# Kernel tuning notes

Measured on AMD Instinct MI355X. Metric: run time of the kernel, lower is better.

## Reference

```python
import jax, jax.numpy as jnp
import numpy as np

D_MODEL = 2048
NUM_HEADS = 16
D_K = D_MODEL // NUM_HEADS


def setup_inputs() -> dict:
    key = jax.random.key(0)
    ks = jax.random.split(key, 9)
    s = 1.0 / np.sqrt(D_MODEL)
    return {
        "x": jax.random.normal(ks[0], (2, 2048, D_MODEL), dtype=jnp.float32),
        "Wq": jax.random.normal(ks[1], (D_MODEL, D_MODEL), dtype=jnp.float32) * s,
        "bq": jax.random.normal(ks[2], (D_MODEL,), dtype=jnp.float32) * 0.01,
        "Wk": jax.random.normal(ks[3], (D_MODEL, D_MODEL), dtype=jnp.float32) * s,
        "bk": jax.random.normal(ks[4], (D_MODEL,), dtype=jnp.float32) * 0.01,
        "Wv": jax.random.normal(ks[5], (D_MODEL, D_MODEL), dtype=jnp.float32) * s,
        "bv": jax.random.normal(ks[6], (D_MODEL,), dtype=jnp.float32) * 0.01,
        "Wo": jax.random.normal(ks[7], (D_MODEL, D_MODEL), dtype=jnp.float32) * s,
        "bo": jax.random.normal(ks[8], (D_MODEL,), dtype=jnp.float32) * 0.01,
    }


def reference(x, Wq, bq, Wk, bk, Wv, bv, Wo, bo):
    B, T, C = x.shape
    H, Dk = NUM_HEADS, D_K
    # projections (torch Linear: y = x @ W^T + b; here weights stored as [in,out])
    q = (x @ Wq + bq).reshape(B, T, H, Dk).transpose(0, 2, 1, 3)  # [B,H,T,Dk]
    k = (x @ Wk + bk).reshape(B, T, H, Dk).transpose(0, 2, 1, 3)
    v = (x @ Wv + bv).reshape(B, T, H, Dk).transpose(0, 2, 1, 3)
    score = jnp.einsum("bhqd,bhkd->bhqk", q, k) / jnp.sqrt(jnp.float32(Dk))
    attn = jax.nn.softmax(score, axis=-1)
    out = jnp.einsum("bhqk,bhkd->bhqd", attn, v)  # [B,H,T,Dk]
    out = out.transpose(0, 2, 1, 3).reshape(B, T, C)
    return out @ Wo + bo
```

## Files before the change

### kernel.cpp

```cpp
#include <hip/hip_runtime.h>
#include <cstdint>

typedef _Float16 f16;
typedef __attribute__((ext_vector_type(4))) _Float16 f16x4;
typedef __attribute__((ext_vector_type(8))) _Float16 f16x8;
typedef __attribute__((ext_vector_type(4))) float f32x4;

#define DM   2048
#define TSEQ 2048
#define NB   2
#define NH   16
#define DKH  128
#define LOG2E 1.44269504088896f

__device__ __forceinline__ void gload_lds16(const void* g, void* l) {
  __builtin_amdgcn_global_load_lds((const __attribute__((address_space(1))) void*)g,
                                   (__attribute__((address_space(3))) void*)l, 16, 0, 0);
}

__global__ __launch_bounds__(256) void cvt_kernel(const float* __restrict__ src,
                                                  f16* __restrict__ dst, int n8) {
  int i = blockIdx.x * 256 + threadIdx.x;
  if (i >= n8) return;
  const float4* s = (const float4*)src + 2 * (size_t)i;
  float4 a = s[0], b = s[1];
  f16x8 o;
  o[0]=(f16)a.x; o[1]=(f16)a.y; o[2]=(f16)a.z; o[3]=(f16)a.w;
  o[4]=(f16)b.x; o[5]=(f16)b.y; o[6]=(f16)b.z; o[7]=(f16)b.w;
  ((f16x8*)dst)[i] = o;
}

__global__ __launch_bounds__(256) void wt_kernel(const float* __restrict__ W0, const float* __restrict__ W1,
                                                 const float* __restrict__ W2, const float* __restrict__ W3,
                                                 f16* __restrict__ Dqkv, f16* __restrict__ Dout) {
  __shared__ f16 S[64 * 80];
  int z = blockIdx.z;
  const float* W = (z == 0) ? W0 : (z == 1) ? W1 : (z == 2) ? W2 : W3;
  f16* D = (z < 3) ? (Dqkv + (size_t)z * DM * DM) : Dout;
  int n0 = blockIdx.x * 64, k0 = blockIdx.y * 64;
  int tid = threadIdx.x;
#pragma unroll
  for (int i = 0; i < 4; i++) {
    int flat = i * 256 + tid;
    int r = flat >> 4, c4 = flat & 15;
    float4 v = *(const float4*)(W + (size_t)(k0 + r) * DM + n0 + c4 * 4);
    S[(c4 * 4 + 0) * 80 + r] = (f16)v.x;
    S[(c4 * 4 + 1) * 80 + r] = (f16)v.y;
    S[(c4 * 4 + 2) * 80 + r] = (f16)v.z;
    S[(c4 * 4 + 3) * 80 + r] = (f16)v.w;
  }
  __syncthreads();
#pragma unroll
  for (int i = 0; i < 2; i++) {
    int flat = i * 256 + tid;
    int nl = flat >> 3, kc = flat & 7;
    f16x8 v = *(const f16x8*)&S[nl * 80 + kc * 8];
    *(f16x8*)(D + (size_t)(n0 + nl) * DM + k0 + kc * 8) = v;
  }
}

template <int MODE>
__global__ __launch_bounds__(256) void gemm_kernel(const f16* __restrict__ A, const f16* __restrict__ Bt,
                                                   const float* __restrict__ b0, const float* __restrict__ b1,
                                                   const float* __restrict__ b2,
                                                   f16* __restrict__ Oh, float* __restrict__ Of) {
  __shared__ f16 As[128 * 32];
  __shared__ f16 Bs[128 * 32];
  const int K = DM;
  int tid = threadIdx.x, l = tid & 63, w = tid >> 6;
  int wm = w >> 1, wn = w & 1;
  int m0 = blockIdx.y * 128, n0 = blockIdx.x * 128;
  f32x4 acc[4][4] = {};

  for (int kt = 0; kt < K / 32; ++kt) {
    __syncthreads();
#pragma unroll
    for (int i = 0; i < 2; i++) {
      int flat = (w * 2 + i) * 64 + l;
      int row = flat >> 2, c = flat & 3;
      int csw = c ^ (row & 3);
      gload_lds16(A  + (size_t)(m0 + row) * K + kt * 32 + csw * 8, &As[(w * 2 + i) * 512]);
      gload_lds16(Bt + (size_t)(n0 + row) * K + kt * 32 + csw * 8, &Bs[(w * 2 + i) * 512]);
    }
    __syncthreads();
    f16x8 af[4], bfr[4];
#pragma unroll
    for (int mi = 0; mi < 4; mi++) {
      int row = wm * 64 + mi * 16 + (l & 15);
      int c = (l >> 4) ^ (row & 3);
      af[mi] = *(const f16x8*)&As[row * 32 + c * 8];
    }
#pragma unroll
    for (int ni = 0; ni < 4; ni++) {
      int row = wn * 64 + ni * 16 + (l & 15);
      int c = (l >> 4) ^ (row & 3);
      bfr[ni] = *(const f16x8*)&Bs[row * 32 + c * 8];
    }
#pragma unroll
    for (int mi = 0; mi < 4; mi++)
#pragma unroll
      for (int ni = 0; ni < 4; ni++)
        acc[mi][ni] = __builtin_amdgcn_mfma_f32_16x16x32_f16(af[mi], bfr[ni], acc[mi][ni], 0, 0, 0);
  }

#pragma unroll
  for (int mi = 0; mi < 4; mi++) {
    int gm = m0 + wm * 64 + mi * 16 + ((l >> 4) << 2);
#pragma unroll
    for (int ni = 0; ni < 4; ni++) {
      int gn = n0 + wn * 64 + ni * 16 + (l & 15);
      if (MODE == 0) {
        int proj = gn >> 11, nn = gn & 2047;
        const float* bp = (proj == 0) ? b0 : (proj == 1) ? b1 : b2;
        float bias = bp[nn];
        int h = nn >> 7, d = nn & 127;
        int b = gm >> 11;
        int t0 = gm & 2047;
        if (proj < 2) {
#pragma unroll
          for (int r = 0; r < 4; r++) {
            Oh[(size_t)proj * ((size_t)NB * NH * TSEQ * DKH) +
               (((size_t)(b * NH + h) * TSEQ + t0 + r) * DKH) + d] = (f16)(acc[mi][ni][r] + bias);
          }
        } else {
          f16x4 pk;
#pragma unroll
          for (int r = 0; r < 4; r++) pk[r] = (f16)(acc[mi][ni][r] + bias);
          *(f16x4*)(Oh + 2ull * ((size_t)NB * NH * TSEQ * DKH) +
                    ((size_t)(b * NH + h) * DKH + d) * TSEQ + t0) = pk;
        }
      } else {
        float bias = b0[gn];
#pragma unroll
        for (int r = 0; r < 4; r++)
          Of[(size_t)(gm + r) * DM + gn] = acc[mi][ni][r] + bias;
      }
    }
  }
}

__global__ __launch_bounds__(256, 2) void attn_kernel(const f16* __restrict__ Qb, const f16* __restrict__ Kb,
                                                      const f16* __restrict__ Vtb, f16* __restrict__ AO) {
  __shared__ f16 Ks[64 * 128];
  __shared__ f16 Vt[128 * 64];
  __shared__ f16 Ps[4][32 * 72];
  int tid = threadIdx.x, l = tid & 63, w = tid >> 6;
  int lo = l & 15, hi = l >> 4;
  int lin = blockIdx.x;
  int xcd = lin & 7, slot = lin >> 3;
  int bh = xcd * 4 + (slot & 3), qt = slot >> 2;
  const float CSC = 0.12753257f;
  const float THR = 62.0f;
  const f16* Qg = Qb + (size_t)bh * TSEQ * DKH;
  const f16* Kg = Kb + (size_t)bh * TSEQ * DKH;
  const f16* Vg = Vtb + (size_t)bh * DKH * TSEQ;

  f16x8 aq[2][4];
#pragma unroll
  for (int hf = 0; hf < 2; hf++) {
    int qrow = qt * 128 + w * 32 + hf * 16 + lo;
#pragma unroll
    for (int c = 0; c < 4; c++)
      aq[hf][c] = *(const f16x8*)(Qg + (size_t)qrow * DKH + c * 32 + (hi << 3));
  }

  f32x4 o[2][8] = {};
  float mrow[2] = {-INFINITY, -INFINITY};
  float lrow[2] = {0.f, 0.f};

  for (int ktile = 0; ktile < TSEQ / 64; ++ktile) {
    __syncthreads();
#pragma unroll
    for (int i = 0; i < 4; i++) {
      int chunk = (w * 4 + i) * 64 + l;
      int rowk = chunk >> 4, c = chunk & 15;
      int csw = c ^ (rowk & 15);
      gload_lds16(Kg + (size_t)(ktile * 64 + rowk) * DKH + csw * 8, &Ks[(w * 4 + i) * 512]);
    }
#pragma unroll
    for (int i = 0; i < 4; i++) {
      int chunk = (w * 4 + i) * 64 + l;
      int d = chunk >> 3, c = chunk & 7;
      int csw = c ^ (d & 7);
      gload_lds16(Vg + (size_t)d * TSEQ + ktile * 64 + csw * 8, &Vt[(w * 4 + i) * 512]);
    }
    __syncthreads();

    f32x4 s[2][4] = {};
    __builtin_amdgcn_s_setprio(1);
#pragma unroll
    for (int ks = 0; ks < 4; ++ks) {
      int ktl = ks * 16 + lo;
#pragma unroll
      for (int c = 0; c < 4; c++) {
        int cc = (c * 4 + hi) ^ lo;
        f16x8 bk = *(const f16x8*)&Ks[ktl * 128 + cc * 8];
        s[0][ks] = __builtin_amdgcn_mfma_f32_16x16x32_f16(bk, aq[0][c], s[0][ks], 0, 0, 0);
        s[1][ks] = __builtin_amdgcn_mfma_f32_16x16x32_f16(bk, aq[1][c], s[1][ks], 0, 0, 0);
      }
    }
    __builtin_amdgcn_s_setprio(0);

#pragma unroll
    for (int hf = 0; hf < 2; hf++) {
      float mk[4];
#pragma unroll
      for (int ks = 0; ks < 4; ks++)
        mk[ks] = fmaxf(fmaxf(s[hf][ks][0], s[hf][ks][1]), fmaxf(s[hf][ks][2], s[hf][ks][3]));
      float mt = fmaxf(fmaxf(mk[0], mk[1]), fmaxf(mk[2], mk[3]));
      mt = fmaxf(mt, __shfl_xor(mt, 16));
      mt = fmaxf(mt, __shfl_xor(mt, 32));

      if (__any(mt > mrow[hf] + THR)) {
        float mn = fmaxf(mrow[hf], mt);
        float al = exp2f((mrow[hf] - mn) * CSC);
        mrow[hf] = mn;
        lrow[hf] *= al;
        float alr[4];
#pragma unroll
        for (int r = 0; r < 4; r++) alr[r] = __shfl(al, (hi << 2) + r);
#pragma unroll
        for (int dsub = 0; dsub < 8; dsub++)
#pragma unroll
          for (int r = 0; r < 4; r++) o[hf][dsub][r] *= alr[r];
      }

      float mCn = -mrow[hf] * CSC;
      float sum = 0.f;
#pragma unroll
      for (int ks = 0; ks < 4; ks++) {
        f16x4 pk;
        float part = 0.f;
#pragma unroll
        for (int r = 0; r < 4; r++) {
          float p = exp2f(__builtin_fmaf(s[hf][ks][r], CSC, mCn));
          pk[r] = (f16)p;
          part += p;
        }
        sum += part;
        *(f16x4*)&Ps[w][(hf * 16 + lo) * 72 + ks * 16 + (hi << 2)] = pk;
      }
      sum += __shfl_xor(sum, 16);
      sum += __shfl_xor(sum, 32);
      lrow[hf] += sum;
    }

    f16x8 pa[2][2];
#pragma unroll
    for (int hf = 0; hf < 2; hf++)
#pragma unroll
      for (int kk = 0; kk < 2; kk++)
        pa[hf][kk] = *(const f16x8*)&Ps[w][(hf * 16 + lo) * 72 + kk * 32 + (hi << 3)];
    __builtin_amdgcn_s_setprio(1);
#pragma unroll
    for (int kk = 0; kk < 2; kk++) {
#pragma unroll
      for (int dsub = 0; dsub < 8; dsub++) {
        int d = dsub * 16 + lo;
        f16x8 vf = *(const f16x8*)&Vt[d * 64 + (((kk * 4 + hi) ^ (d & 7)) << 3)];
        o[0][dsub] = __builtin_amdgcn_mfma_f32_16x16x32_f16(pa[0][kk], vf, o[0][dsub], 0, 0, 0);
        o[1][dsub] = __builtin_amdgcn_mfma_f32_16x16x32_f16(pa[1][kk], vf, o[1][dsub], 0, 0, 0);
      }
    }
    __builtin_amdgcn_s_setprio(0);
  }

  int b = bh >> 4, h = bh & 15;
#pragma unroll
  for (int hf = 0; hf < 2; hf++) {
    float inv = 1.0f / lrow[hf];
    float invr[4];
#pragma unroll
    for (int r = 0; r < 4; r++) invr[r] = __shfl(inv, (hi << 2) + r);
#pragma unroll
    for (int r = 0; r < 4; r++) {
      int t = qt * 128 + w * 32 + hf * 16 + (hi << 2) + r;
      f16* dst = AO + ((size_t)b * TSEQ + t) * DM + h * DKH;
#pragma unroll
      for (int dsub = 0; dsub < 8; dsub++)
        dst[dsub * 16 + lo] = (f16)(o[hf][dsub][r] * invr[r]);
    }
  }
}

extern "C" void kernel_launch(void* const* d_in, const int* in_sizes, int n_in,
                              void* d_out, int out_size, void* d_ws, size_t ws_size,
                              hipStream_t stream) {
  const float* x  = (const float*)d_in[0];
  const float* Wq = (const float*)d_in[1];
  const float* bq = (const float*)d_in[2];
  const float* Wk = (const float*)d_in[3];
  const float* bk = (const float*)d_in[4];
  const float* Wv = (const float*)d_in[5];
  const float* bv = (const float*)d_in[6];
  const float* Wo = (const float*)d_in[7];
  const float* bo = (const float*)d_in[8];

  f16* ws    = (f16*)d_ws;
  f16* xb    = ws;
  f16* WtQKV = ws + 8388608ull;
  f16* WtO   = ws + 20971520ull;
  f16* Q     = ws + 25165824ull;
  f16* Kp    = ws + 33554432ull;
  f16* Vp    = ws + 41943040ull;
  f16* AO    = xb;

  cvt_kernel<<<4096, 256, 0, stream>>>(x, xb, (NB * TSEQ * DM) / 8);
  wt_kernel<<<dim3(32, 32, 4), 256, 0, stream>>>(Wq, Wk, Wv, Wo, WtQKV, WtO);
  gemm_kernel<0><<<dim3(48, 32), 256, 0, stream>>>(xb, WtQKV, bq, bk, bv, Q, nullptr);
  attn_kernel<<<512, 256, 0, stream>>>(Q, Kp, Vp, AO);
  gemm_kernel<1><<<dim3(16, 32), 256, 0, stream>>>(AO, WtO, bo, nullptr, nullptr, nullptr, (float*)d_out);
}
```

Before: 285.8 us.

## Rewrite GEMM as 256x128 double-buffered pipelined kernel with XCD-aware tile swizzle

Replaces the simple single-buffered 128x128, K=32 GEMM with a 512-thread, 256x128 tile, K=64 kernel. It double-buffers LDS and interleaves global-to-LDS staging with per-quarter MFMA phases, using manual s_barrier, waitcnt and setprio. The block index is remapped so neighbouring tiles land on the same XCD for L2 reuse. This targets the load/compute serialization and barrier stalls of the old loop, at the cost of more LDS per block (96KB), fragile hand-placed wait counts, and redundant tail loads.

```diff
diff --git a/kernel.cpp b/kernel.cpp
--- a/kernel.cpp
+++ b/kernel.cpp
@@ -17,6 +17,9 @@
   __builtin_amdgcn_global_load_lds((const __attribute__((address_space(1))) void*)g,
                                    (__attribute__((address_space(3))) void*)l, 16, 0, 0);
 }
+
+#define SBAR()  asm volatile("s_barrier" ::: "memory")
+#define LGKM0() { asm volatile("s_waitcnt lgkmcnt(0)" ::: "memory"); __builtin_amdgcn_sched_barrier(0); }
 
 __global__ __launch_bounds__(256) void cvt_kernel(const float* __restrict__ src,
                                                   f16* __restrict__ dst, int n8) {
@@ -60,47 +63,138 @@
 }
 
 template <int MODE>
-__global__ __launch_bounds__(256) void gemm_kernel(const f16* __restrict__ A, const f16* __restrict__ Bt,
-                                                   const float* __restrict__ b0, const float* __restrict__ b1,
-                                                   const float* __restrict__ b2,
-                                                   f16* __restrict__ Oh, float* __restrict__ Of) {
-  __shared__ f16 As[128 * 32];
-  __shared__ f16 Bs[128 * 32];
+__global__ __launch_bounds__(512, 2) void gemm_kernel(const f16* __restrict__ A, const f16* __restrict__ Bt,
+                                                      const float* __restrict__ b0, const float* __restrict__ b1,
+                                                      const float* __restrict__ b2,
+                                                      f16* __restrict__ Oh, float* __restrict__ Of) {
+  __shared__ __align__(16) f16 As[2][256 * 64];
+  __shared__ __align__(16) f16 Bs[2][128 * 64];
   const int K = DM;
+  const int NT = K / 64;
+  const int NITER = NT / 2;
+  const int NXB = (MODE == 0) ? 48 : 16;
+  const int CPX = (MODE == 0) ? 96 : 32;
   int tid = threadIdx.x, l = tid & 63, w = tid >> 6;
+  int lo = l & 15, hi = l >> 4;
   int wm = w >> 1, wn = w & 1;
-  int m0 = blockIdx.y * 128, n0 = blockIdx.x * 128;
+  int lin = blockIdx.x;
+  int swz = (lin & 7) * CPX + (lin >> 3);
+  int bx = swz % NXB, by = swz / NXB;
+  int m0 = by * 256, n0 = bx * 128;
+
+  const f16* Ag = A + (size_t)m0 * K;
+  const f16* Bg = Bt + (size_t)n0 * K;
+
+  auto stageA = [&](int b, int h, int t) {
+#pragma unroll
+    for (int i = 0; i < 2; i++) {
+      int flat = i * 512 + tid;
+      int row = flat >> 3, c = flat & 7;
+      int csw = c ^ (row & 7);
+      gload_lds16(Ag + (size_t)(h * 128 + row) * K + t * 64 + csw * 8,
+                  &As[b][h * 8192 + i * 4096 + w * 512]);
+    }
+  };
+  auto stageB = [&](int b, int t) {
+#pragma unroll
+    for (int i = 0; i < 2; i++) {
+      int flat = i * 512 + tid;
+      int row = flat >> 3, c = flat & 7;
+      int csw = c ^ (row & 7);
+      gload_lds16(Bg + (size_t)row * K + t * 64 + csw * 8,
+                  &Bs[b][i * 4096 + w * 512]);
+    }
+  };
+
   f32x4 acc[4][4] = {};
-
-  for (int kt = 0; kt < K / 32; ++kt) {
-    __syncthreads();
-#pragma unroll
-    for (int i = 0; i < 2; i++) {
-      int flat = (w * 2 + i) * 64 + l;
-      int row = flat >> 2, c = flat & 3;
-      int csw = c ^ (row & 3);
-      gload_lds16(A  + (size_t)(m0 + row) * K + kt * 32 + csw * 8, &As[(w * 2 + i) * 512]);
-      gload_lds16(Bt + (size_t)(n0 + row) * K + kt * 32 + csw * 8, &Bs[(w * 2 + i) * 512]);
-    }
-    __syncthreads();
-    f16x8 af[4], bfr[4];
-#pragma unroll
-    for (int mi = 0; mi < 4; mi++) {
-      int row = wm * 64 + mi * 16 + (l & 15);
-      int c = (l >> 4) ^ (row & 3);
-      af[mi] = *(const f16x8*)&As[row * 32 + c * 8];
-    }
-#pragma unroll
-    for (int ni = 0; ni < 4; ni++) {
-      int row = wn * 64 + ni * 16 + (l & 15);
-      int c = (l >> 4) ^ (row & 3);
-      bfr[ni] = *(const f16x8*)&Bs[row * 32 + c * 8];
-    }
-#pragma unroll
-    for (int mi = 0; mi < 4; mi++)
-#pragma unroll
-      for (int ni = 0; ni < 4; ni++)
-        acc[mi][ni] = __builtin_amdgcn_mfma_f32_16x16x32_f16(af[mi], bfr[ni], acc[mi][ni], 0, 0, 0);
+  f16x8 bfr[4][2];
+
+#define READ_BFRAGS(b)                                                          \
+  {                                                                             \
+    _Pragma("unroll")                                                           \
+    for (int ni = 0; ni < 4; ni++) {                                            \
+      int row = wn * 64 + ni * 16 + lo;                                         \
+      bfr[ni][0] = *(const f16x8*)&Bs[b][row * 64 + (((0 + hi) ^ (row & 7)) << 3)]; \
+      bfr[ni][1] = *(const f16x8*)&Bs[b][row * 64 + (((4 + hi) ^ (row & 7)) << 3)]; \
+    }                                                                           \
+  }
+
+#define PHASE_HEAD(bq, q)                                                       \
+    f16x8 af0, af1;                                                             \
+    {                                                                           \
+      int row = wm * 64 + (q) * 16 + lo;                                        \
+      af0 = *(const f16x8*)&As[bq][row * 64 + (((0 + hi) ^ (row & 7)) << 3)];   \
+      af1 = *(const f16x8*)&As[bq][row * 64 + (((4 + hi) ^ (row & 7)) << 3)];   \
+    }
+
+#define PHASE_MFMA(q)                                                           \
+    __builtin_amdgcn_s_setprio(1);                                              \
+    _Pragma("unroll")                                                           \
+    for (int ni = 0; ni < 4; ni++) {                                            \
+      acc[q][ni] = __builtin_amdgcn_mfma_f32_16x16x32_f16(af0, bfr[ni][0], acc[q][ni], 0, 0, 0); \
+      acc[q][ni] = __builtin_amdgcn_mfma_f32_16x16x32_f16(af1, bfr[ni][1], acc[q][ni], 0, 0, 0); \
+    }                                                                           \
+    __builtin_amdgcn_s_setprio(0);
+
+  stageB(0, 0);
+  stageA(0, 0, 0);
+  stageA(0, 1, 0);
+  stageB(1, 1);
+  asm volatile("s_waitcnt vmcnt(2)" ::: "memory");
+  SBAR();
+
+#pragma unroll 1
+  for (int it = 0; it < NITER; ++it) {
+    int t1  = 2 * it + 1;
+    int tn0 = (2 * it + 2 < NT) ? 2 * it + 2 : NT - 1;
+    int tn1 = (2 * it + 3 < NT) ? 2 * it + 3 : NT - 1;
+
+    {
+      READ_BFRAGS(0);
+      PHASE_HEAD(0, 0);
+      stageA(1, 0, t1);
+      asm volatile("s_waitcnt lgkmcnt(8)" ::: "memory");
+      SBAR(); LGKM0(); PHASE_MFMA(0); SBAR();
+    }
+    {
+      PHASE_HEAD(0, 1);
+      stageA(1, 1, t1);
+      SBAR(); LGKM0(); PHASE_MFMA(1); SBAR();
+    }
+    {
+      PHASE_HEAD(0, 2);
+      stageB(0, tn0);
+      SBAR(); LGKM0(); PHASE_MFMA(2); SBAR();
+    }
+    {
+      PHASE_HEAD(0, 3);
+      SBAR(); LGKM0(); PHASE_MFMA(3);
+      asm volatile("s_waitcnt vmcnt(2)" ::: "memory");
+      SBAR();
+    }
+    {
+      READ_BFRAGS(1);
+      PHASE_HEAD(1, 0);
+      stageA(0, 0, tn0);
+      asm volatile("s_waitcnt lgkmcnt(8)" ::: "memory");
+      SBAR(); LGKM0(); PHASE_MFMA(0); SBAR();
+    }
+    {
+      PHASE_HEAD(1, 1);
+      stageA(0, 1, tn0);
+      SBAR(); LGKM0(); PHASE_MFMA(1); SBAR();
+    }
+    {
+      PHASE_HEAD(1, 2);
+      stageB(1, tn1);
+      SBAR(); LGKM0(); PHASE_MFMA(2); SBAR();
+    }
+    {
+      PHASE_HEAD(1, 3);
+      SBAR(); LGKM0(); PHASE_MFMA(3);
+      asm volatile("s_waitcnt vmcnt(2)" ::: "memory");
+      SBAR();
+    }
   }
 
 #pragma unroll
@@ -137,6 +231,10 @@
       }
     }
   }
+  asm volatile("s_waitcnt vmcnt(0)" ::: "memory");
+#undef READ_BFRAGS
+#undef PHASE_HEAD
+#undef PHASE_MFMA
 }
 
 __global__ __launch_bounds__(256, 2) void attn_kernel(const f16* __restrict__ Qb, const f16* __restrict__ Kb,
@@ -307,7 +405,7 @@
 
   cvt_kernel<<<4096, 256, 0, stream>>>(x, xb, (NB * TSEQ * DM) / 8);
   wt_kernel<<<dim3(32, 32, 4), 256, 0, stream>>>(Wq, Wk, Wv, Wo, WtQKV, WtO);
-  gemm_kernel<0><<<dim3(48, 32), 256, 0, stream>>>(xb, WtQKV, bq, bk, bv, Q, nullptr);
+  gemm_kernel<0><<<768, 512, 0, stream>>>(xb, WtQKV, bq, bk, bv, Q, nullptr);
   attn_kernel<<<512, 256, 0, stream>>>(Q, Kp, Vp, AO);
-  gemm_kernel<1><<<dim3(16, 32), 256, 0, stream>>>(AO, WtO, bo, nullptr, nullptr, nullptr, (float*)d_out);
-}
+  gemm_kernel<1><<<256, 512, 0, stream>>>(AO, WtO, bo, nullptr, nullptr, nullptr, (float*)d_out);
+}
```

Result: no change. 290.2 us (+1.5%).
